# Kernel tuning notes

Measured on AMD Instinct MI355X. Metric: run time of the kernel, lower is better.

The kernel has to match this reference:

```python
import jax, jax.numpy as jnp
import numpy as np

NUM_HEADS = 8
EPS = 1e-6


def setup_inputs() -> dict:
    key = jax.random.key(0)
    ks = jax.random.split(key, 6)
    B, T, E = 2, 4096, 512
    s = 0.02
    x = jax.random.normal(ks[0], (B, T, E), dtype=jnp.float32)
    Wq = jax.random.normal(ks[1], (E, E), dtype=jnp.float32) * s
    Wk = jax.random.normal(ks[2], (E, E), dtype=jnp.float32) * s
    Wv = jax.random.normal(ks[3], (E, E), dtype=jnp.float32) * s
    Wo = jax.random.normal(ks[4], (E, E), dtype=jnp.float32) * s
    bq = jnp.zeros((E,), jnp.float32)
    bk = jnp.zeros((E,), jnp.float32)
    bv = jnp.zeros((E,), jnp.float32)
    bo = jnp.zeros((E,), jnp.float32)
    return {"x": x, "Wq": Wq, "bq": bq, "Wk": Wk, "bk": bk,
            "Wv": Wv, "bv": bv, "Wo": Wo, "bo": bo}


def _linear(x, W, b):
    # torch nn.Linear: y = x @ W.T + b
    return x @ W.T + b


def _feature_map(x):
    return jax.nn.elu(x) + 1.0


def _linear_attention(x, Wq, bq, Wk, bk, Wv, bv, Wo, bo):
    B, T, E = x.shape
    H = NUM_HEADS
    D = E // H

    def heads(y):  # (B,T,E) -> (T,B,H,D), time-major for scan
        return y.reshape(B, T, H, D).transpose(1, 0, 2, 3)

    q = _feature_map(heads(_linear(x, Wq, bq)))
    k = _feature_map(heads(_linear(x, Wk, bk)))
    v = heads(_linear(x, Wv, bv))

    # Causal linear attention: running KV outer-product state S (B,H,D,D)
    # and running key sum z (B,H,D). Equivalent to the naive
    # cumsum-of-outer-products (B,H,T,D,D) formulation, but O(D^2) state.
    S0 = jnp.zeros((B, H, D, D), x.dtype)
    z0 = jnp.zeros((B, H, D), x.dtype)

    def step(carry, qkv):
        S, z = carry
        qt, kt, vt = qkv  # each (B,H,D)
        S = S + kt[..., :, None] * vt[..., None, :]
        z = z + kt
        num = jnp.einsum('bhd,bhde->bhe', qt, S)
        den = jnp.sum(qt * z, axis=-1) + EPS  # (B,H)
        return (S, z), num / den[..., None]

    _, out = jax.lax.scan(step, (S0, z0), (q, k, v))  # (T,B,H,D)
    out = out.transpose(1, 0, 2, 3).reshape(B, T, E)
    return _linear(out, Wo, bo)


def reference(x, Wq, bq, Wk, bk, Wv, bv, Wo, bo):
    return _linear_attention(x, Wq, bq, Wk, bk, Wv, bv, Wo, bo)
```

## Files before the change

kernel.cpp:

```cpp
#include <hip/hip_runtime.h>
#include <hip/hip_bf16.h>

#define T_SEQ 4096
#define EMB   512
#define NH    8
#define HD    64
#define BATCH 2
#define M_ROWS (BATCH * T_SEQ)
#define NCHUNK 64
#define CS     64
#define BHEADS (BATCH * NH)

using bf16 = __hip_bfloat16;
typedef __attribute__((ext_vector_type(8))) short short8;
typedef __attribute__((ext_vector_type(4))) float floatx4;

__device__ __forceinline__ float bs2f(short s) {
    return __uint_as_float(((unsigned)(unsigned short)s) << 16);
}
__device__ __forceinline__ short f2bs(float f) {
    bf16 h = __float2bfloat16(f);
    return *reinterpret_cast<short*>(&h);
}
__device__ __forceinline__ float load_elem(const bf16* p, size_t i) {
    return __bfloat162float(p[i]);
}
__device__ __forceinline__ void stage8(const bf16* g, short* l) {
    *reinterpret_cast<short8*>(l) = *reinterpret_cast<const short8*>(g);
}
__device__ __forceinline__ void stage8(const float* g, short* l) {
    float4 a = *reinterpret_cast<const float4*>(g);
    float4 b = *reinterpret_cast<const float4*>(g + 4);
    short8 v;
    v[0] = f2bs(a.x); v[1] = f2bs(a.y); v[2] = f2bs(a.z); v[3] = f2bs(a.w);
    v[4] = f2bs(b.x); v[5] = f2bs(b.y); v[6] = f2bs(b.z); v[7] = f2bs(b.w);
    *reinterpret_cast<short8*>(l) = v;
}

__device__ __forceinline__ void gload_lds16(const short* g, short* l) {
    __builtin_amdgcn_global_load_lds(
        (const __attribute__((address_space(1))) void*)g,
        (__attribute__((address_space(3))) void*)l, 16, 0, 0);
}

#define LDSTR 72

__device__ __forceinline__ int probe_mode(const void* x) {
    const uint4* p = (const uint4*)x;
    const int tid = threadIdx.x & 255;
    bool bad = false;
    #pragma unroll
    for (int i = 0; i < 2; ++i) {
        uint4 u = p[tid + i * 256];
        const unsigned w[4] = {u.x, u.y, u.z, u.w};
        #pragma unroll
        for (int k = 0; k < 4; ++k) {
            const float f = __uint_as_float(w[k] << 16);
            if (!(fabsf(f) <= 1e9f)) bad = true;
        }
    }
    return __syncthreads_or(bad ? 1 : 0) ? 1 : 0;
}

template <typename T>
__device__ __forceinline__ void convert_body(
    const void* const* in, short* xb, short* Wb, short* bb, int c)
{
    if (c < 524288) {
        stage8((const T*)in[0] + (size_t)c * 8, xb + (size_t)c * 8);
    } else if (c < 655360) {
        const int c2 = c - 524288;
        const int w = c2 >> 15;
        const int off = (c2 & 32767) * 8;
        const T* src = (const T*)in[w == 0 ? 1 : (w == 1 ? 3 : (w == 2 ? 5 : 7))];
        stage8(src + off, Wb + w * 262144 + off);
    } else if (c < 655616) {
        const int c3 = c - 655360;
        const int bsel = c3 >> 6;
        const int off = (c3 & 63) * 8;
        const T* src = (const T*)in[bsel == 0 ? 2 : (bsel == 1 ? 4 : (bsel == 2 ? 6 : 8))];
        stage8(src + off, bb + bsel * 512 + off);
    }
}

__global__ __launch_bounds__(256) void convert_all(
    const void* x, const void* Wq, const void* bq,
    const void* Wk, const void* bk, const void* Wv, const void* bv,
    const void* Wo, const void* bo,
    short* __restrict__ xb, short* __restrict__ Wb, short* __restrict__ bb)
{
    const void* in[9] = {x, Wq, bq, Wk, bk, Wv, bv, Wo, bo};
    const int mode = probe_mode(x);
    const int c = blockIdx.x * 256 + threadIdx.x;
    if (mode) convert_body<float>(in, xb, Wb, bb, c);
    else      convert_body<bf16>(in, xb, Wb, bb, c);
}

__global__ __launch_bounds__(512) void qkv_gemm_dl(
    const short* __restrict__ xb, const short* __restrict__ Wb,
    const short* __restrict__ bb,
    bf16* __restrict__ Qf, bf16* __restrict__ Kf, bf16* __restrict__ Vf)
{
    const int mtile = blockIdx.x;
    const int ntile = blockIdx.y;
    const int which = ntile >> 2;
    const short* W = Wb + (size_t)which * 262144;
    const bf16* bias = (const bf16*)(bb + which * 512);
    bf16* outp = (which == 0) ? Qf : ((which == 1) ? Kf : Vf);
    const int nbase = (ntile & 3) * 128;
    const int mbase = mtile * 256;

    __shared__ short As[256 * 64];
    __shared__ short Bs[128 * 64];

    const int tid  = threadIdx.x;
    const int wave = tid >> 6, lane = tid & 63;
    const int wm = wave >> 1, wn = wave & 1;
    const int lm = lane & 15, quad = lane >> 4;
    const int srow = lane >> 3;
    const int scol = (lane & 7) * 8;

    floatx4 acc[4][4];
    const floatx4 zero = {0.f, 0.f, 0.f, 0.f};
    #pragma unroll
    for (int mt = 0; mt < 4; ++mt)
        #pragma unroll
        for (int nt = 0; nt < 4; ++nt) acc[mt][nt] = zero;

    for (int kt = 0; kt < EMB; kt += 64) {
        #pragma unroll
        for (int j = 0; j < 4; ++j) {
            const int issue = wave * 4 + j;
            const int row = issue * 8 + srow;
            gload_lds16(xb + (size_t)(mbase + row) * EMB + kt + scol,
                        &As[issue * 512]);
        }
        #pragma unroll
        for (int j = 0; j < 2; ++j) {
            const int issue = wave * 2 + j;
            const int row = issue * 8 + srow;
            gload_lds16(W + (size_t)(nbase + row) * EMB + kt + scol,
                        &Bs[issue * 512]);
        }
        __syncthreads();
        #pragma unroll
        for (int ks = 0; ks < 2; ++ks) {
            short8 af[4], bfr[4];
            #pragma unroll
            for (int mt = 0; mt < 4; ++mt)
                af[mt] = *reinterpret_cast<const short8*>(
                    &As[(wm * 64 + mt * 16 + lm) * 64 + ks * 32 + quad * 8]);
            #pragma unroll
            for (int nt = 0; nt < 4; ++nt)
                bfr[nt] = *reinterpret_cast<const short8*>(
                    &Bs[(wn * 64 + nt * 16 + lm) * 64 + ks * 32 + quad * 8]);
            #pragma unroll
            for (int mt = 0; mt < 4; ++mt)
                #pragma unroll
                for (int nt = 0; nt < 4; ++nt)
                    acc[mt][nt] = __builtin_amdgcn_mfma_f32_16x16x32_bf16(
                        af[mt], bfr[nt], acc[mt][nt], 0, 0, 0);
        }
        __syncthreads();
    }

    #pragma unroll
    for (int nt = 0; nt < 4; ++nt) {
        const int col = nbase + wn * 64 + nt * 16 + lm;
        const float bv_ = load_elem(bias, col & 511);
        const int h = col >> 6, d = col & 63;
        #pragma unroll
        for (int mt = 0; mt < 4; ++mt)
            #pragma unroll
            for (int r = 0; r < 4; ++r) {
                const int row = mbase + wm * 64 + mt * 16 + quad * 4 + r;
                const int b = row >> 12, t = row & (T_SEQ - 1);
                float v = acc[mt][nt][r] + bv_;
                if (which != 2) v = (v > 0.f) ? (v + 1.f) : __expf(v);
                outp[(((size_t)(b * NH + h)) * T_SEQ + t) * HD + d] = __float2bfloat16(v);
            }
    }
}

__global__ __launch_bounds__(256) void chunk_kv(
    const bf16* __restrict__ Kf, const bf16* __restrict__ Vf,
    float* __restrict__ KVt, float* __restrict__ ksum)
{
    const int bh = blockIdx.x >> 6;
    const int c  = blockIdx.x & 63;
    __shared__ short Kt[64 * LDSTR];
    __shared__ short Vt[64 * LDSTR];
    const int tid = threadIdx.x;
    const bf16* kp = Kf + ((size_t)bh * T_SEQ + c * CS) * HD;
    const bf16* vp = Vf + ((size_t)bh * T_SEQ + c * CS) * HD;

    #pragma unroll
    for (int j = 0; j < 2; ++j) {
        const int u = j * 256 + tid;
        const int e0 = u * 8;
        const int s = e0 >> 6, d0 = e0 & 63;
        short8 ku = *reinterpret_cast<const short8*>(kp + e0);
        short8 vu = *reinterpret_cast<const short8*>(vp + e0);
        #pragma unroll
        for (int i = 0; i < 8; ++i) {
            Kt[(d0 + i) * LDSTR + s] = ku[i];
            Vt[(d0 + i) * LDSTR + s] = vu[i];
        }
    }
    __syncthreads();

    const int w = tid >> 6, lane = tid & 63;
    const int lm = lane & 15, quad = lane >> 4;

    floatx4 acc[4];
    const floatx4 zero = {0.f, 0.f, 0.f, 0.f};
    #pragma unroll
    for (int nt = 0; nt < 4; ++nt) acc[nt] = zero;

    #pragma unroll
    for (int ks = 0; ks < 2; ++ks) {
        short8 av = *reinterpret_cast<const short8*>(
            &Vt[(w * 16 + lm) * LDSTR + ks * 32 + quad * 8]);
        #pragma unroll
        for (int nt = 0; nt < 4; ++nt) {
            short8 bk = *reinterpret_cast<const short8*>(
                &Kt[(nt * 16 + lm) * LDSTR + ks * 32 + quad * 8]);
            acc[nt] = __builtin_amdgcn_mfma_f32_16x16x32_bf16(av, bk, acc[nt], 0, 0, 0);
        }
    }

    float* kvout = KVt + ((size_t)bh * NCHUNK + c) * 4096;
    #pragma unroll
    for (int nt = 0; nt < 4; ++nt)
        #pragma unroll
        for (int r = 0; r < 4; ++r)
            kvout[(w * 16 + quad * 4 + r) * 64 + nt * 16 + lm] = acc[nt][r];

    if (tid < 64) {
        float s = 0.f;
        #pragma unroll 8
        for (int t = 0; t < 64; ++t) s += bs2f(Kt[tid * LDSTR + t]);
        ksum[((size_t)bh * NCHUNK + c) * 64 + tid] = s;
    }
}

__global__ __launch_bounds__(256) void prefix_kv(
    const float* __restrict__ KVt, bf16* __restrict__ KVb,
    float* __restrict__ ksum)
{
    const int bh   = blockIdx.x >> 4;
    const int part = blockIdx.x & 15;
    const int tid  = threadIdx.x;
    const int e    = part * 256 + tid;
    const float* src = KVt + (size_t)bh * NCHUNK * 4096 + e;
    bf16* dst = KVb + (size_t)bh * NCHUNK * 4096 + e;

    float s = 0.f;
    #pragma unroll
    for (int cb = 0; cb < 2; ++cb) {
        float v[32];
        #pragma unroll
        for (int i = 0; i < 32; ++i) v[i] = src[(size_t)(cb * 32 + i) * 4096];
        #pragma unroll
        for (int i = 0; i < 32; ++i) {
            dst[(size_t)(cb * 32 + i) * 4096] = __float2bfloat16(s);
            s += v[i];
        }
    }

    if (part == 0 && tid < 64) {
        float* zb = ksum + (size_t)bh * NCHUNK * 64 + tid;
        float z = 0.f;
        #pragma unroll
        for (int cb = 0; cb < 4; ++cb) {
            float zv[16];
            #pragma unroll
            for (int i = 0; i < 16; ++i) zv[i] = zb[(size_t)(cb * 16 + i) * 64];
            #pragma unroll
            for (int i = 0; i < 16; ++i) {
                zb[(size_t)(cb * 16 + i) * 64] = z;
                z += zv[i];
            }
        }
    }
}

__global__ __launch_bounds__(256, 4) void attn_mfma(
    const bf16* __restrict__ Qf, const bf16* __restrict__ Kf,
    const bf16* __restrict__ Vf, const bf16* __restrict__ KVb,
    const float* __restrict__ ksum, bf16* __restrict__ Of)
{
    const int bh = blockIdx.x >> 6;
    const int c  = blockIdx.x & 63;
    const int b  = bh >> 3, h = bh & 7;

    __shared__ short Qs [64 * LDSTR];
    __shared__ short Ksn[64 * LDSTR];
    __shared__ short Vt [64 * LDSTR];
    __shared__ short Ps [64 * LDSTR];
    __shared__ float zprev[64];

    const int tid = threadIdx.x;
    const int w = tid >> 6, lane = tid & 63;
    const int lm = lane & 15, quad = lane >> 4;
    const size_t coff = ((size_t)bh * T_SEQ + c * CS) * HD;
    const bf16* Sb = KVb + ((size_t)bh * NCHUNK + c) * 4096;

    #pragma unroll
    for (int j = 0; j < 2; ++j) {
        const int u  = j * 256 + tid;
        const int e0 = u * 8;
        const int r = e0 >> 6, cc = e0 & 63;
        *reinterpret_cast<short8*>(&Qs [r * LDSTR + cc]) =
            *reinterpret_cast<const short8*>(Qf + coff + e0);
        *reinterpret_cast<short8*>(&Ksn[r * LDSTR + cc]) =
            *reinterpret_cast<const short8*>(Kf + coff + e0);
        short8 vu = *reinterpret_cast<const short8*>(Vf + coff + e0);
        #pragma unroll
        for (int i = 0; i < 8; ++i) Vt[(cc + i) * LDSTR + r] = vu[i];
    }
    if (tid < 64) zprev[tid] = ksum[((size_t)bh * NCHUNK + c) * 64 + tid];
    __syncthreads();

    const floatx4 zero = {0.f, 0.f, 0.f, 0.f};
    short8 aq[2];
    #pragma unroll
    for (int ks = 0; ks < 2; ++ks)
        aq[ks] = *reinterpret_cast<const short8*>(
            &Qs[(w * 16 + lm) * LDSTR + ks * 32 + quad * 8]);

    floatx4 pacc[4];
    #pragma unroll
    for (int nt = 0; nt < 4; ++nt) pacc[nt] = zero;
    #pragma unroll
    for (int ks = 0; ks < 2; ++ks)
        #pragma unroll
        for (int nt = 0; nt < 4; ++nt) {
            short8 bk = *reinterpret_cast<const short8*>(
                &Ksn[(nt * 16 + lm) * LDSTR + ks * 32 + quad * 8]);
            pacc[nt] = __builtin_amdgcn_mfma_f32_16x16x32_bf16(aq[ks], bk, pacc[nt], 0, 0, 0);
        }

    float tot[4] = {0.f, 0.f, 0.f, 0.f};
    #pragma unroll
    for (int nt = 0; nt < 4; ++nt)
        #pragma unroll
        for (int r = 0; r < 4; ++r) {
            const int t = w * 16 + quad * 4 + r;
            const int s = nt * 16 + lm;
            const float m = (s <= t) ? pacc[nt][r] : 0.f;
            Ps[t * LDSTR + s] = f2bs(m);
            tot[r] += m;
        }
    #pragma unroll
    for (int r = 0; r < 4; ++r) {
        const int t = w * 16 + quad * 4 + r;
        #pragma unroll
        for (int j = 0; j < 4; ++j) {
            const int d = lm + j * 16;
            tot[r] += bs2f(Qs[t * LDSTR + d]) * zprev[d];
        }
    }
    #pragma unroll
    for (int mask = 1; mask < 16; mask <<= 1)
        #pragma unroll
        for (int r = 0; r < 4; ++r) tot[r] += __shfl_xor(tot[r], mask);
    float rdenl[4];
    #pragma unroll
    for (int r = 0; r < 4; ++r) rdenl[r] = 1.f / (tot[r] + 1e-6f);

    floatx4 oacc[4];
    #pragma unroll
    for (int nt = 0; nt < 4; ++nt) oacc[nt] = zero;
    #pragma unroll
    for (int ks = 0; ks < 2; ++ks)
        #pragma unroll
        for (int nt = 0; nt < 4; ++nt) {
            short8 bs = *reinterpret_cast<const short8*>(
                Sb + (nt * 16 + lm) * 64 + ks * 32 + quad * 8);
            oacc[nt] = __builtin_amdgcn_mfma_f32_16x16x32_bf16(aq[ks], bs, oacc[nt], 0, 0, 0);
        }

    #pragma unroll
    for (int ks = 0; ks < 2; ++ks) {
        short8 ap = *reinterpret_cast<const short8*>(
            &Ps[(w * 16 + lm) * LDSTR + ks * 32 + quad * 8]);
        #pragma unroll
        for (int nt = 0; nt < 4; ++nt) {
            short8 bv = *reinterpret_cast<const short8*>(
                &Vt[(nt * 16 + lm) * LDSTR + ks * 32 + quad * 8]);
            oacc[nt] = __builtin_amdgcn_mfma_f32_16x16x32_bf16(ap, bv, oacc[nt], 0, 0, 0);
        }
    }

    #pragma unroll
    for (int nt = 0; nt < 4; ++nt)
        #pragma unroll
        for (int r = 0; r < 4; ++r) {
            const int t  = w * 16 + quad * 4 + r;
            const int dv = nt * 16 + lm;
            const int tg = c * CS + t;
            Of[((size_t)(b * T_SEQ + tg)) * EMB + h * HD + dv] =
                __float2bfloat16(oacc[nt][r] * rdenl[r]);
        }
}

__global__ __launch_bounds__(256) void out_proj_dl(
    const void* __restrict__ xprobe,
    const short* __restrict__ A, const short* __restrict__ Wb,
    const short* __restrict__ bb, void* __restrict__ out)
{
    const int mode = probe_mode(xprobe);

    const int mbase = blockIdx.x * 128;
    const int nbase = blockIdx.y * 128;
    const short* W = Wb + (size_t)3 * 262144;
    const bf16* bias = (const bf16*)(bb + 3 * 512);

    __shared__ short As[128 * 64];
    __shared__ short Bs[128 * 64];

    const int tid  = threadIdx.x;
    const int wave = tid >> 6, lane = tid & 63;
    const int wm = wave >> 1, wn = wave & 1;
    const int lm = lane & 15, quad = lane >> 4;
    const int srow = lane >> 3;
    const int scol = (lane & 7) * 8;

    floatx4 acc[4][4];
    const floatx4 zero = {0.f, 0.f, 0.f, 0.f};
    #pragma unroll
    for (int mt = 0; mt < 4; ++mt)
        #pragma unroll
        for (int nt = 0; nt < 4; ++nt) acc[mt][nt] = zero;

    for (int kt = 0; kt < EMB; kt += 64) {
        #pragma unroll
        for (int j = 0; j < 4; ++j) {
            const int issue = wave * 4 + j;
            const int row = issue * 8 + srow;
            gload_lds16(A + (size_t)(mbase + row) * EMB + kt + scol,
                        &As[issue * 512]);
            gload_lds16(W + (size_t)(nbase + row) * EMB + kt + scol,
                        &Bs[issue * 512]);
        }
        __syncthreads();
        #pragma unroll
        for (int ks = 0; ks < 2; ++ks) {
            short8 af[4], bfr[4];
            #pragma unroll
            for (int mt = 0; mt < 4; ++mt)
                af[mt] = *reinterpret_cast<const short8*>(
                    &As[(wm * 64 + mt * 16 + lm) * 64 + ks * 32 + quad * 8]);
            #pragma unroll
            for (int nt = 0; nt < 4; ++nt)
                bfr[nt] = *reinterpret_cast<const short8*>(
                    &Bs[(wn * 64 + nt * 16 + lm) * 64 + ks * 32 + quad * 8]);
            #pragma unroll
            for (int mt = 0; mt < 4; ++mt)
                #pragma unroll
                for (int nt = 0; nt < 4; ++nt)
                    acc[mt][nt] = __builtin_amdgcn_mfma_f32_16x16x32_bf16(
                        af[mt], bfr[nt], acc[mt][nt], 0, 0, 0);
        }
        __syncthreads();
    }

    #pragma unroll
    for (int nt = 0; nt < 4; ++nt) {
        const int col = nbase + wn * 64 + nt * 16 + lm;
        const float bv_ = load_elem(bias, col);
        #pragma unroll
        for (int mt = 0; mt < 4; ++mt)
            #pragma unroll
            for (int r = 0; r < 4; ++r) {
                const int row = mbase + wm * 64 + mt * 16 + quad * 4 + r;
                const float v = acc[mt][nt][r] + bv_;
                if (mode) ((float*)out)[(size_t)row * EMB + col] = v;
                else      ((bf16*)out)[(size_t)row * EMB + col] = __float2bfloat16(v);
            }
    }
}

extern "C" void kernel_launch(void* const* d_in, const int* in_sizes, int n_in,
                              void* d_out, int out_size, void* d_ws, size_t ws_size,
                              hipStream_t stream)
{
    bf16* Qf = (bf16*)((char*)d_ws + 64);
    bf16* Kf = Qf + 4194304;
    bf16* Vf = Kf + 4194304;
    float* KVt = (float*)(Vf + 4194304);
    short* xb = (short*)KVt;
    float* ks = KVt + 4194304;
    bf16* Of = (bf16*)(ks + 65536);
    short* Wb = (short*)(Of + 4194304);
    short* bb = Wb + 1048576;
    bf16* KVb = (bf16*)(bb + 2048);

    convert_all<<<dim3(2561), 256, 0, stream>>>(
        d_in[0], d_in[1], d_in[2], d_in[3], d_in[4],
        d_in[5], d_in[6], d_in[7], d_in[8], xb, Wb, bb);

    qkv_gemm_dl<<<dim3(32, 12), 512, 0, stream>>>(xb, Wb, bb, Qf, Kf, Vf);
    chunk_kv<<<dim3(BHEADS * NCHUNK), 256, 0, stream>>>(Kf, Vf, KVt, ks);
    prefix_kv<<<dim3(BHEADS * 16), 256, 0, stream>>>(KVt, KVb, ks);
    attn_mfma<<<dim3(BHEADS * NCHUNK), 256, 0, stream>>>(Qf, Kf, Vf, KVb, ks, Of);

    out_proj_dl<<<dim3(64, 4), 256, 0, stream>>>(
        d_in[0], (const short*)Of, Wb, bb, d_out);
}
```

Before: 153.9 us.

## Double-buffer LDS in QKV and output GEMMs, widen QKV N-tile to 192

Both GEMM kernels now use two LDS buffers so the next K-slice's global-to-LDS loads are issued before computing on the current slice, and one barrier per iteration is dropped. The QKV GEMM now treats Q/K/V weights as one concatenated 1536-wide matrix with 192-column tiles, which cuts the grid from 32x12 to 32x8 blocks and gives each wave a 4x6 MFMA tile. The Q/K/V destination and bias are chosen per column in the epilogue. The cost is doubled LDS use (about 112KB for the QKV kernel) and more accumulator registers, which lowers occupancy, and the 256-block grid may underfill the CUs.

```diff
diff --git a/kernel.cpp b/kernel.cpp
--- a/kernel.cpp
+++ b/kernel.cpp
@@ -101,17 +101,11 @@
     const short* __restrict__ bb,
     bf16* __restrict__ Qf, bf16* __restrict__ Kf, bf16* __restrict__ Vf)
 {
-    const int mtile = blockIdx.x;
-    const int ntile = blockIdx.y;
-    const int which = ntile >> 2;
-    const short* W = Wb + (size_t)which * 262144;
-    const bf16* bias = (const bf16*)(bb + which * 512);
-    bf16* outp = (which == 0) ? Qf : ((which == 1) ? Kf : Vf);
-    const int nbase = (ntile & 3) * 128;
-    const int mbase = mtile * 256;
-
-    __shared__ short As[256 * 64];
-    __shared__ short Bs[128 * 64];
+    const int mbase = blockIdx.x * 256;
+    const int nbase = blockIdx.y * 192;
+
+    __shared__ short As[2][256 * 64];
+    __shared__ short Bs[2][192 * 64];
 
     const int tid  = threadIdx.x;
     const int wave = tid >> 6, lane = tid & 63;
@@ -120,55 +114,66 @@
     const int srow = lane >> 3;
     const int scol = (lane & 7) * 8;
 
-    floatx4 acc[4][4];
+    floatx4 acc[4][6];
     const floatx4 zero = {0.f, 0.f, 0.f, 0.f};
     #pragma unroll
     for (int mt = 0; mt < 4; ++mt)
         #pragma unroll
-        for (int nt = 0; nt < 4; ++nt) acc[mt][nt] = zero;
-
-    for (int kt = 0; kt < EMB; kt += 64) {
+        for (int nt = 0; nt < 6; ++nt) acc[mt][nt] = zero;
+
+    auto stage = [&](int buf, int kt) {
         #pragma unroll
         for (int j = 0; j < 4; ++j) {
             const int issue = wave * 4 + j;
             const int row = issue * 8 + srow;
             gload_lds16(xb + (size_t)(mbase + row) * EMB + kt + scol,
-                        &As[issue * 512]);
-        }
-        #pragma unroll
-        for (int j = 0; j < 2; ++j) {
-            const int issue = wave * 2 + j;
+                        &As[buf][issue * 512]);
+        }
+        #pragma unroll
+        for (int j = 0; j < 3; ++j) {
+            const int issue = wave * 3 + j;
             const int row = issue * 8 + srow;
-            gload_lds16(W + (size_t)(nbase + row) * EMB + kt + scol,
-                        &Bs[issue * 512]);
-        }
-        __syncthreads();
+            gload_lds16(Wb + (size_t)(nbase + row) * EMB + kt + scol,
+                        &Bs[buf][issue * 512]);
+        }
+    };
+
+    stage(0, 0);
+    __syncthreads();
+
+    #pragma unroll 2
+    for (int step = 0; step < 8; ++step) {
+        const int cur = step & 1;
+        if (step < 7) stage(cur ^ 1, (step + 1) * 64);
         #pragma unroll
         for (int ks = 0; ks < 2; ++ks) {
-            short8 af[4], bfr[4];
+            short8 af[4], bfr[6];
             #pragma unroll
             for (int mt = 0; mt < 4; ++mt)
                 af[mt] = *reinterpret_cast<const short8*>(
-                    &As[(wm * 64 + mt * 16 + lm) * 64 + ks * 32 + quad * 8]);
-            #pragma unroll
-            for (int nt = 0; nt < 4; ++nt)
+                    &As[cur][(wm * 64 + mt * 16 + lm) * 64 + ks * 32 + quad * 8]);
+            #pragma unroll
+            for (int nt = 0; nt < 6; ++nt)
                 bfr[nt] = *reinterpret_cast<const short8*>(
-                    &Bs[(wn * 64 + nt * 16 + lm) * 64 + ks * 32 + quad * 8]);
+                    &Bs[cur][(wn * 96 + nt * 16 + lm) * 64 + ks * 32 + quad * 8]);
             #pragma unroll
             for (int mt = 0; mt < 4; ++mt)
                 #pragma unroll
-                for (int nt = 0; nt < 4; ++nt)
+                for (int nt = 0; nt < 6; ++nt)
                     acc[mt][nt] = __builtin_amdgcn_mfma_f32_16x16x32_bf16(
                         af[mt], bfr[nt], acc[mt][nt], 0, 0, 0);
         }
-        __syncthreads();
-    }
-
-    #pragma unroll
-    for (int nt = 0; nt < 4; ++nt) {
-        const int col = nbase + wn * 64 + nt * 16 + lm;
-        const float bv_ = load_elem(bias, col & 511);
-        const int h = col >> 6, d = col & 63;
+        if (step < 7) __syncthreads();
+    }
+
+    #pragma unroll
+    for (int nt = 0; nt < 6; ++nt) {
+        const int col = nbase + wn * 96 + nt * 16 + lm;
+        const int which = col >> 9;
+        const int cw = col & 511;
+        const float bv_ = load_elem((const bf16*)bb, col);
+        const int h = cw >> 6, d = cw & 63;
+        bf16* outp = (which == 0) ? Qf : ((which == 1) ? Kf : Vf);
         #pragma unroll
         for (int mt = 0; mt < 4; ++mt)
             #pragma unroll
@@ -417,8 +422,8 @@
     const short* W = Wb + (size_t)3 * 262144;
     const bf16* bias = (const bf16*)(bb + 3 * 512);
 
-    __shared__ short As[128 * 64];
-    __shared__ short Bs[128 * 64];
+    __shared__ short As[2][128 * 64];
+    __shared__ short Bs[2][128 * 64];
 
     const int tid  = threadIdx.x;
     const int wave = tid >> 6, lane = tid & 63;
@@ -434,28 +439,36 @@
         #pragma unroll
         for (int nt = 0; nt < 4; ++nt) acc[mt][nt] = zero;
 
-    for (int kt = 0; kt < EMB; kt += 64) {
+    auto stage = [&](int buf, int kt) {
         #pragma unroll
         for (int j = 0; j < 4; ++j) {
             const int issue = wave * 4 + j;
             const int row = issue * 8 + srow;
             gload_lds16(A + (size_t)(mbase + row) * EMB + kt + scol,
-                        &As[issue * 512]);
+                        &As[buf][issue * 512]);
             gload_lds16(W + (size_t)(nbase + row) * EMB + kt + scol,
-                        &Bs[issue * 512]);
-        }
-        __syncthreads();
+                        &Bs[buf][issue * 512]);
+        }
+    };
+
+    stage(0, 0);
+    __syncthreads();
+
+    #pragma unroll 2
+    for (int step = 0; step < 8; ++step) {
+        const int cur = step & 1;
+        if (step < 7) stage(cur ^ 1, (step + 1) * 64);
         #pragma unroll
         for (int ks = 0; ks < 2; ++ks) {
             short8 af[4], bfr[4];
             #pragma unroll
             for (int mt = 0; mt < 4; ++mt)
                 af[mt] = *reinterpret_cast<const short8*>(
-                    &As[(wm * 64 + mt * 16 + lm) * 64 + ks * 32 + quad * 8]);
+                    &As[cur][(wm * 64 + mt * 16 + lm) * 64 + ks * 32 + quad * 8]);
             #pragma unroll
             for (int nt = 0; nt < 4; ++nt)
                 bfr[nt] = *reinterpret_cast<const short8*>(
-                    &Bs[(wn * 64 + nt * 16 + lm) * 64 + ks * 32 + quad * 8]);
+                    &Bs[cur][(wn * 64 + nt * 16 + lm) * 64 + ks * 32 + quad * 8]);
             #pragma unroll
             for (int mt = 0; mt < 4; ++mt)
                 #pragma unroll
@@ -463,7 +476,7 @@
                     acc[mt][nt] = __builtin_amdgcn_mfma_f32_16x16x32_bf16(
                         af[mt], bfr[nt], acc[mt][nt], 0, 0, 0);
         }
-        __syncthreads();
+        if (step < 7) __syncthreads();
     }
 
     #pragma unroll
@@ -501,7 +514,7 @@
         d_in[0], d_in[1], d_in[2], d_in[3], d_in[4],
         d_in[5], d_in[6], d_in[7], d_in[8], xb, Wb, bb);
 
-    qkv_gemm_dl<<<dim3(32, 12), 512, 0, stream>>>(xb, Wb, bb, Qf, Kf, Vf);
+    qkv_gemm_dl<<<dim3(32, 8), 512, 0, stream>>>(xb, Wb, bb, Qf, Kf, Vf);
     chunk_kv<<<dim3(BHEADS * NCHUNK), 256, 0, stream>>>(Kf, Vf, KVt, ks);
     prefix_kv<<<dim3(BHEADS * 16), 256, 0, stream>>>(KVt, KVb, ks);
     attn_mfma<<<dim3(BHEADS * NCHUNK), 256, 0, stream>>>(Qf, Kf, Vf, KVb, ks, Of);
```

New measurement: 154.7 us. No clear change (+0.5%).
